# Kernel tuning notes

Measured on AMD Instinct MI355X. Metric: run time of the kernel, lower is better.

The kernel has to match this reference:

```python
import jax, jax.numpy as jnp
import numpy as np

L = 9  # local window size


def local_windows(x, l):
    # x: (n, c, h, w) -> (n, c, l*l, h, w): all l*l shifted views (zero-padded),
    # equivalent to F.unfold(x, kernel=(l,l), stride=1, padding=l//2).
    n, c, h, w = x.shape
    pad = l // 2
    xp = jnp.pad(x, ((0, 0), (0, 0), (pad, pad), (pad, pad)))
    views = [xp[:, :, i:i + h, j:j + w] for i in range(l) for j in range(l)]
    return jnp.stack(views, axis=2)


def setup_inputs() -> dict:
    key = jax.random.key(0)
    k1, k2, k3 = jax.random.split(key, 3)
    n, c, h, w = 2, 128, 64, 64
    ft = jax.random.normal(k1, (n, c, h, w), dtype=jnp.float32)
    fk = jax.random.normal(k2, (n, c, h, w), dtype=jnp.float32)
    # 1x1 conv weight shared between key and query projections: (out_c, in_c)
    W = jax.random.normal(k3, (128, 128), dtype=jnp.float32) * (1.0 / np.sqrt(128))
    return {"ft": ft, "fk": fk, "W": W}


def reference(ft, fk, W):
    # 1x1 conv == channel matmul
    key = jnp.einsum('oi,nihw->nohw', W, ft)    # key from frame t
    query = jnp.einsum('oi,nihw->nohw', W, fk)  # query from frame k
    # f_similar(query, key, L): per-pixel query dotted with L*L local keys
    key_win = local_windows(key, L)             # (n, c, L*L, h, w)
    sim = jnp.einsum('nchw,nckhw->nhwk', query, key_win)  # (n, h, w, L*L)
    weight = jax.nn.softmax(sim, axis=-1)
    # f_weighting(ft, weight, L): weighted sum of L*L local raw-ft vectors
    ft_win = local_windows(ft, L)                # (n, c, L*L, h, w)
    out = jnp.einsum('nckhw,nhwk->nchw', ft_win, weight)
    return out
```

## Files before the change

kernel.cpp:

```cpp
#include <hip/hip_runtime.h>
#include <hip/hip_bf16.h>


#define Hh 64
#define Ww 64
#define Cc 128
#define Nn 2
#define KK 81
#define HW (Hh * Ww)
#define CHW (Cc * HW)
#define P_TOT (Nn * HW)

typedef _Float16 h8 __attribute__((ext_vector_type(8)));
typedef _Float16 h4 __attribute__((ext_vector_type(4)));
typedef float f4v __attribute__((ext_vector_type(4)));

#ifndef __has_builtin
#define __has_builtin(x) 0
#endif

#if __has_builtin(__builtin_amdgcn_ds_read_tr16_b64_v4f16)
#define TR_BUILTIN 1
typedef __fp16 g4 __attribute__((__vector_size__(4 * sizeof(__fp16))));
static __device__ __forceinline__ h4 tr16(const _Float16* p) {
    g4 r = __builtin_amdgcn_ds_read_tr16_b64_v4f16(
        (__attribute__((address_space(3))) g4*)p);
    return __builtin_bit_cast(h4, r);
}
#else
#define TR_BUILTIN 0
static __device__ __forceinline__ h4 tr16(const _Float16* p) {
    h4 r;
    asm volatile("ds_read_b64_tr_b16 %0, %1"
                 : "=v"(r)
                 : "v"((__attribute__((address_space(3))) _Float16*)p));
    return r;
}
#endif

__global__ __launch_bounds__(256) void proj_kernel(const float* __restrict__ ft,
                                                   const float* __restrict__ fk,
                                                   const float* __restrict__ Wm,
                                                   _Float16* __restrict__ Qbuf,
                                                   _Float16* __restrict__ Kbuf,
                                                   _Float16* __restrict__ fth) {
    __shared__ __align__(16) _Float16 Wth[128 * 136];
    __shared__ __align__(16) _Float16 xkh[32 * 136];
    __shared__ __align__(16) _Float16 xqh[32 * 136];
    const int t = threadIdx.x;
    const int p0 = blockIdx.x * 32;
    const int nn = p0 >> 12;
    const int gbase = nn * CHW + (p0 & 4095);

#pragma unroll 4
    for (int e = t; e < 4096; e += 256) {
        const int n = e >> 5, ch = e & 31;
        const float4 v = *(const float4*)&Wm[n * 128 + (ch << 2)];
        h4 hv; hv[0] = (_Float16)v.x; hv[1] = (_Float16)v.y;
               hv[2] = (_Float16)v.z; hv[3] = (_Float16)v.w;
        *(h4*)&Wth[n * 136 + (ch << 2)] = hv;
    }
#pragma unroll 4
    for (int e = t; e < 1024; e += 256) {
        const int c = e >> 3, pc = e & 7;
        const float4 vk = *(const float4*)&ft[gbase + c * HW + (pc << 2)];
        const float4 vq = *(const float4*)&fk[gbase + c * HW + (pc << 2)];
        const int px = pc << 2;
        xkh[(px    ) * 136 + c] = (_Float16)vk.x;
        xkh[(px + 1) * 136 + c] = (_Float16)vk.y;
        xkh[(px + 2) * 136 + c] = (_Float16)vk.z;
        xkh[(px + 3) * 136 + c] = (_Float16)vk.w;
        xqh[(px    ) * 136 + c] = (_Float16)vq.x;
        xqh[(px + 1) * 136 + c] = (_Float16)vq.y;
        xqh[(px + 2) * 136 + c] = (_Float16)vq.z;
        xqh[(px + 3) * 136 + c] = (_Float16)vq.w;
    }
    __syncthreads();

#pragma unroll
    for (int e = t; e < 512; e += 256) {
        const int px = e >> 4, cq = e & 15;
        *(h8*)&fth[(size_t)(p0 + px) * 128 + (cq << 3)] =
            *(const h8*)&xkh[px * 136 + (cq << 3)];
    }

    const int lane = t & 63, wv = t >> 6;
    const int quad = lane >> 4, l15 = lane & 15;
    const _Float16* xs = (wv >> 1) ? xqh : xkh;
    _Float16* dst = (wv >> 1) ? Qbuf : Kbuf;
    const int mt = wv & 1;
    const int abase = (mt * 16 + l15) * 136 + (quad << 3);
    const h8 a0 = *(const h8*)&xs[abase];
    const h8 a1 = *(const h8*)&xs[abase + 32];
    const h8 a2 = *(const h8*)&xs[abase + 64];
    const h8 a3 = *(const h8*)&xs[abase + 96];
#pragma unroll
    for (int nt = 0; nt < 8; ++nt) {
        const int bbase = (nt * 16 + l15) * 136 + (quad << 3);
        const h8 b0 = *(const h8*)&Wth[bbase];
        const h8 b1 = *(const h8*)&Wth[bbase + 32];
        const h8 b2 = *(const h8*)&Wth[bbase + 64];
        const h8 b3 = *(const h8*)&Wth[bbase + 96];
        f4v acc = {0.f, 0.f, 0.f, 0.f};
        acc = __builtin_amdgcn_mfma_f32_16x16x32_f16(a0, b0, acc, 0, 0, 0);
        acc = __builtin_amdgcn_mfma_f32_16x16x32_f16(a1, b1, acc, 0, 0, 0);
        acc = __builtin_amdgcn_mfma_f32_16x16x32_f16(a2, b2, acc, 0, 0, 0);
        acc = __builtin_amdgcn_mfma_f32_16x16x32_f16(a3, b3, acc, 0, 0, 0);
        const int col = nt * 16 + l15;
        const size_t rb = (size_t)(p0 + mt * 16 + (quad << 2)) * 128 + col;
#pragma unroll
        for (int r = 0; r < 4; ++r)
            dst[rb + (size_t)r * 128] = (_Float16)acc[r];
    }
}

#define FTL_CH 2312
__global__ __launch_bounds__(256, 4) void sim_weight_kernel(const _Float16* __restrict__ Qbuf,
                                                            const _Float16* __restrict__ Kbuf,
                                                            const _Float16* __restrict__ fth,
                                                            float* __restrict__ out) {
    __shared__ __align__(16) unsigned char smem[40720];
    _Float16* Ksw  = (_Float16*)smem;
    _Float16* Qsw  = (_Float16*)(smem + 36864);
    _Float16* ftl  = (_Float16*)smem;
    float*    simbF= (float*)smem;
    _Float16* simb = (_Float16*)(smem + 39168);
    float*    redM = (float*)(smem + 40464);
    float*    redS = (float*)(smem + 40592);

    const int t  = threadIdx.x;
    const int b  = blockIdx.x;
    const int x0 = (b & 7) << 3;
    const int y  = (b >> 3) & 63;
    const int nn = b >> 9;
    const int pg0 = (nn << 12) + (y << 6) + x0;

#pragma unroll 3
    for (int e = t; e < 144 * 16; e += 256) {
        const int v = e >> 4, ci = e & 15;
        const int gx = x0 + (v & 15) - 4;
        const int gy = y + (v >> 4) - 4;
        h8 val = {0, 0, 0, 0, 0, 0, 0, 0};
        if ((unsigned)gx < 64u && (unsigned)gy < 64u)
            val = *(const h8*)&Kbuf[(size_t)((nn << 12) + (gy << 6) + gx) * 128 + (ci << 3)];
        *(h8*)&Ksw[(v << 7) + ((ci ^ (v & 15)) << 3)] = val;
    }
    if (t < 128) {
        const int v = t >> 4, ci = t & 15;
        *(h8*)&Qsw[(v << 7) + ((ci ^ v) << 3)] =
            *(const h8*)&Qbuf[(size_t)(pg0 + v) * 128 + (ci << 3)];
    }
    __syncthreads();

    h8 pf[9];
#pragma unroll
    for (int i = 0; i < 9; ++i) {
        const int e = t + (i << 8);
        const int v = e >> 4, ci = e & 15;
        const int gx = x0 + (v & 15) - 4;
        const int gy = y + (v >> 4) - 4;
        h8 val = {0, 0, 0, 0, 0, 0, 0, 0};
        if ((unsigned)gx < 64u && (unsigned)gy < 64u)
            val = *(const h8*)&fth[(size_t)((nn << 12) + (gy << 6) + gx) * 128 + (ci << 3)];
        pf[i] = val;
    }

    const int lane = t & 63, wv = t >> 6;
    const int quad = lane >> 4, l15 = lane & 15;
    const int qrow = l15 & 7;
    h8 qb[4];
#pragma unroll
    for (int kc = 0; kc < 4; ++kc) {
        const int ci = (kc << 2) + quad;
        qb[kc] = *(const h8*)&Qsw[(qrow << 7) + ((ci ^ qrow) << 3)];
    }
    const int r0 = wv, r1 = wv + 4;
    f4v acc0 = {0.f,0.f,0.f,0.f}, acc1 = acc0, acc2 = acc0;
#pragma unroll
    for (int kc = 0; kc < 4; ++kc) {
        const int ci = (kc << 2) + quad;
        const h8 kA = *(const h8*)&Ksw[(((r0 << 4) + l15) << 7) + ((ci ^ l15) << 3)];
        const h8 kB = *(const h8*)&Ksw[(((r1 << 4) + l15) << 7) + ((ci ^ l15) << 3)];
        const h8 kC = *(const h8*)&Ksw[(((8  << 4) + l15) << 7) + ((ci ^ l15) << 3)];
        acc0 = __builtin_amdgcn_mfma_f32_16x16x32_f16(kA, qb[kc], acc0, 0, 0, 0);
        acc1 = __builtin_amdgcn_mfma_f32_16x16x32_f16(kB, qb[kc], acc1, 0, 0, 0);
        acc2 = __builtin_amdgcn_mfma_f32_16x16x32_f16(kC, qb[kc], acc2, 0, 0, 0);
    }
    __syncthreads();

#pragma unroll
    for (int reg = 0; reg < 4; ++reg) {
        const int xx = (quad << 2) + reg;
        const int dx = xx - l15;
        const bool ok = (l15 < 8) && (dx >= 0) && (dx < 9);
        if (ok)            simbF[(r0 * 9 + dx) * 8 + l15] = acc0[reg];
        if (ok)            simbF[(r1 * 9 + dx) * 8 + l15] = acc1[reg];
        if (ok && wv == 0) simbF[(8  * 9 + dx) * 8 + l15] = acc2[reg];
    }
    __syncthreads();

    const int p = t & 7, kb = t >> 3;
    const bool has2 = (kb + 64 < KK);
    const float s0 = simbF[kb * 8 + p];
    const float s1 = simbF[(kb + 32) * 8 + p];
    const float s2 = has2 ? simbF[(kb + 64) * 8 + p] : 0.f;
    __syncthreads();

#pragma unroll
    for (int i = 0; i < 9; ++i) {
        const int e = t + (i << 8);
        const int v = e >> 4, ci = e & 15;
        *(h8*)&ftl[(ci >> 1) * FTL_CH + (v << 4) + ((ci & 1) << 3)] = pf[i];
    }

    float m = fmaxf(s0, s1);
    if (has2) m = fmaxf(m, s2);
#pragma unroll
    for (int off = 8; off <= 32; off <<= 1) m = fmaxf(m, __shfl_xor(m, off));
    if ((t & 56) == 0) redM[((t >> 6) << 3) + p] = m;
    __syncthreads();

    const _Float16* ftc0 = ftl + wv * FTL_CH;
    const _Float16* ftc1 = ftl + (wv + 4) * FTL_CH;
    h4 bfr[18];
#pragma unroll
    for (int r = 0; r < 9; ++r) {
        bfr[r]     = tr16(ftc0 + (r << 8) + (lane << 2));
        bfr[9 + r] = tr16(ftc1 + (r << 8) + (lane << 2));
    }

    float mm = fmaxf(fmaxf(redM[p], redM[8 + p]), fmaxf(redM[16 + p], redM[24 + p]));
    const float e0 = __expf(s0 - mm);
    const float e1 = __expf(s1 - mm);
    const float e2 = has2 ? __expf(s2 - mm) : 0.f;
    simb[kb * 8 + p] = (_Float16)e0;
    simb[(kb + 32) * 8 + p] = (_Float16)e1;
    if (has2) simb[(kb + 64) * 8 + p] = (_Float16)e2;
    float s = e0 + e1 + e2;
#pragma unroll
    for (int off = 8; off <= 32; off <<= 1) s += __shfl_xor(s, off);
    if ((t & 56) == 0) redS[((t >> 6) << 3) + p] = s;
    __syncthreads();

#if !TR_BUILTIN
    asm volatile("s_waitcnt lgkmcnt(0)");
    __builtin_amdgcn_sched_barrier(0);
#endif

    f4v aw0 = {0.f, 0.f, 0.f, 0.f}, aw1 = aw0;
#pragma unroll
    for (int r = 0; r < 9; ++r) {
        h4 afr;
#pragma unroll
        for (int j = 0; j < 4; ++j) {
            const int dx = (quad << 2) + j - qrow;
            const bool ok = (unsigned)dx < 9u;
            afr[j] = ok ? simb[(((r * 9 + dx) << 3) + qrow)] : (_Float16)0.f;
        }
        aw0 = __builtin_amdgcn_mfma_f32_16x16x16f16(afr, bfr[r],     aw0, 0, 0, 0);
        aw1 = __builtin_amdgcn_mfma_f32_16x16x16f16(afr, bfr[9 + r], aw1, 0, 0, 0);
    }

    if (quad < 2) {
        const int q4 = quad << 2;
        const float4 rs0 = *(const float4*)&redS[q4];
        const float4 rs1 = *(const float4*)&redS[8 + q4];
        const float4 rs2 = *(const float4*)&redS[16 + q4];
        const float4 rs3 = *(const float4*)&redS[24 + q4];
        const float iv0 = 1.f / (rs0.x + rs1.x + rs2.x + rs3.x);
        const float iv1 = 1.f / (rs0.y + rs1.y + rs2.y + rs3.y);
        const float iv2 = 1.f / (rs0.z + rs1.z + rs2.z + rs3.z);
        const float iv3 = 1.f / (rs0.w + rs1.w + rs2.w + rs3.w);
        const int xb = (y << 6) + x0 + q4;
        const size_t ob0 = ((size_t)((nn << 7) + (wv << 4) + l15) << 12) + xb;
        const size_t ob1 = ((size_t)((nn << 7) + ((wv + 4) << 4) + l15) << 12) + xb;
        float4 o0, o1;
        o0.x = aw0[0] * iv0; o0.y = aw0[1] * iv1; o0.z = aw0[2] * iv2; o0.w = aw0[3] * iv3;
        o1.x = aw1[0] * iv0; o1.y = aw1[1] * iv1; o1.z = aw1[2] * iv2; o1.w = aw1[3] * iv3;
        *(float4*)&out[ob0] = o0;
        *(float4*)&out[ob1] = o1;
    }
}

extern "C" void kernel_launch(void* const* d_in, const int* in_sizes, int n_in,
                              void* d_out, int out_size, void* d_ws, size_t ws_size,
                              hipStream_t stream) {
    const float* ft = (const float*)d_in[0];
    const float* fk = (const float*)d_in[1];
    const float* Wm = (const float*)d_in[2];
    float* out = (float*)d_out;

    _Float16* wsh  = (_Float16*)d_ws;
    _Float16* Qbuf = wsh;
    _Float16* Kbuf = wsh + 1048576;
    _Float16* fth  = wsh + 2097152;

    proj_kernel<<<256, 256, 0, stream>>>(ft, fk, Wm, Qbuf, Kbuf, fth);
    sim_weight_kernel<<<1024, 256, 0, stream>>>(Qbuf, Kbuf, fth, out);
}
```

Before: 77.25 us.

## Compute softmax from MFMA registers and halve projection tile per block

The similarity kernel now computes the softmax max and exp-sum straight from the MFMA accumulator registers, reducing across lanes with shuffles and a small cross-wave array. This drops the fp32 staging buffer and two block barriers. Separately, the projection kernel handles 16 pixels per block instead of 32 and splits output column tiles across waves, launching twice as many blocks to fill more CUs. The trade-off is that each projection block reloads the full weight matrix for half as much work.

```diff
diff --git a/kernel.cpp b/kernel.cpp
--- a/kernel.cpp
+++ b/kernel.cpp
@@ -45,10 +45,10 @@
                                                    _Float16* __restrict__ Kbuf,
                                                    _Float16* __restrict__ fth) {
     __shared__ __align__(16) _Float16 Wth[128 * 136];
-    __shared__ __align__(16) _Float16 xkh[32 * 136];
-    __shared__ __align__(16) _Float16 xqh[32 * 136];
+    __shared__ __align__(16) _Float16 xkh[16 * 136];
+    __shared__ __align__(16) _Float16 xqh[16 * 136];
     const int t = threadIdx.x;
-    const int p0 = blockIdx.x * 32;
+    const int p0 = blockIdx.x * 16;
     const int nn = p0 >> 12;
     const int gbase = nn * CHW + (p0 & 4095);
 
@@ -60,9 +60,9 @@
                hv[2] = (_Float16)v.z; hv[3] = (_Float16)v.w;
         *(h4*)&Wth[n * 136 + (ch << 2)] = hv;
     }
-#pragma unroll 4
-    for (int e = t; e < 1024; e += 256) {
-        const int c = e >> 3, pc = e & 7;
+#pragma unroll
+    for (int e = t; e < 512; e += 256) {
+        const int c = e >> 2, pc = e & 3;
         const float4 vk = *(const float4*)&ft[gbase + c * HW + (pc << 2)];
         const float4 vq = *(const float4*)&fk[gbase + c * HW + (pc << 2)];
         const int px = pc << 2;
@@ -77,9 +77,8 @@
     }
     __syncthreads();
 
-#pragma unroll
-    for (int e = t; e < 512; e += 256) {
-        const int px = e >> 4, cq = e & 15;
+    {
+        const int px = t >> 4, cq = t & 15;
         *(h8*)&fth[(size_t)(p0 + px) * 128 + (cq << 3)] =
             *(const h8*)&xkh[px * 136 + (cq << 3)];
     }
@@ -88,14 +87,15 @@
     const int quad = lane >> 4, l15 = lane & 15;
     const _Float16* xs = (wv >> 1) ? xqh : xkh;
     _Float16* dst = (wv >> 1) ? Qbuf : Kbuf;
-    const int mt = wv & 1;
-    const int abase = (mt * 16 + l15) * 136 + (quad << 3);
+    const int nt0 = (wv & 1) << 2;
+    const int abase = l15 * 136 + (quad << 3);
     const h8 a0 = *(const h8*)&xs[abase];
     const h8 a1 = *(const h8*)&xs[abase + 32];
     const h8 a2 = *(const h8*)&xs[abase + 64];
     const h8 a3 = *(const h8*)&xs[abase + 96];
 #pragma unroll
-    for (int nt = 0; nt < 8; ++nt) {
+    for (int ni = 0; ni < 4; ++ni) {
+        const int nt = nt0 + ni;
         const int bbase = (nt * 16 + l15) * 136 + (quad << 3);
         const h8 b0 = *(const h8*)&Wth[bbase];
         const h8 b1 = *(const h8*)&Wth[bbase + 32];
@@ -107,7 +107,7 @@
         acc = __builtin_amdgcn_mfma_f32_16x16x32_f16(a2, b2, acc, 0, 0, 0);
         acc = __builtin_amdgcn_mfma_f32_16x16x32_f16(a3, b3, acc, 0, 0, 0);
         const int col = nt * 16 + l15;
-        const size_t rb = (size_t)(p0 + mt * 16 + (quad << 2)) * 128 + col;
+        const size_t rb = (size_t)(p0 + (quad << 2)) * 128 + col;
 #pragma unroll
         for (int r = 0; r < 4; ++r)
             dst[rb + (size_t)r * 128] = (_Float16)acc[r];
@@ -123,7 +123,6 @@
     _Float16* Ksw  = (_Float16*)smem;
     _Float16* Qsw  = (_Float16*)(smem + 36864);
     _Float16* ftl  = (_Float16*)smem;
-    float*    simbF= (float*)smem;
     _Float16* simb = (_Float16*)(smem + 39168);
     float*    redM = (float*)(smem + 40464);
     float*    redS = (float*)(smem + 40592);
@@ -186,24 +185,20 @@
         acc1 = __builtin_amdgcn_mfma_f32_16x16x32_f16(kB, qb[kc], acc1, 0, 0, 0);
         acc2 = __builtin_amdgcn_mfma_f32_16x16x32_f16(kC, qb[kc], acc2, 0, 0, 0);
     }
-    __syncthreads();
-
+
+    float m = -3.0e38f;
 #pragma unroll
     for (int reg = 0; reg < 4; ++reg) {
-        const int xx = (quad << 2) + reg;
-        const int dx = xx - l15;
-        const bool ok = (l15 < 8) && (dx >= 0) && (dx < 9);
-        if (ok)            simbF[(r0 * 9 + dx) * 8 + l15] = acc0[reg];
-        if (ok)            simbF[(r1 * 9 + dx) * 8 + l15] = acc1[reg];
-        if (ok && wv == 0) simbF[(8  * 9 + dx) * 8 + l15] = acc2[reg];
-    }
-    __syncthreads();
-
-    const int p = t & 7, kb = t >> 3;
-    const bool has2 = (kb + 64 < KK);
-    const float s0 = simbF[kb * 8 + p];
-    const float s1 = simbF[(kb + 32) * 8 + p];
-    const float s2 = has2 ? simbF[(kb + 64) * 8 + p] : 0.f;
+        const int dx = (quad << 2) + reg - l15;
+        const bool ok = (l15 < 8) && ((unsigned)dx < 9u);
+        if (ok) {
+            m = fmaxf(m, fmaxf(acc0[reg], acc1[reg]));
+            m = fmaxf(m, acc2[reg]);
+        }
+    }
+    m = fmaxf(m, __shfl_xor(m, 16));
+    m = fmaxf(m, __shfl_xor(m, 32));
+    if (quad == 0 && l15 < 8) redM[(wv << 3) + l15] = m;
     __syncthreads();
 
 #pragma unroll
@@ -213,11 +208,24 @@
         *(h8*)&ftl[(ci >> 1) * FTL_CH + (v << 4) + ((ci & 1) << 3)] = pf[i];
     }
 
-    float m = fmaxf(s0, s1);
-    if (has2) m = fmaxf(m, s2);
-#pragma unroll
-    for (int off = 8; off <= 32; off <<= 1) m = fmaxf(m, __shfl_xor(m, off));
-    if ((t & 56) == 0) redM[((t >> 6) << 3) + p] = m;
+    const float mm = fmaxf(fmaxf(redM[qrow], redM[8 + qrow]),
+                           fmaxf(redM[16 + qrow], redM[24 + qrow]));
+    float ssum = 0.f;
+#pragma unroll
+    for (int reg = 0; reg < 4; ++reg) {
+        const int dx = (quad << 2) + reg - l15;
+        const bool ok = (l15 < 8) && ((unsigned)dx < 9u);
+        const float e0 = ok ? __expf(acc0[reg] - mm) : 0.f;
+        const float e1 = ok ? __expf(acc1[reg] - mm) : 0.f;
+        const float e2 = (ok && wv == 0) ? __expf(acc2[reg] - mm) : 0.f;
+        if (ok)            simb[((r0 * 9 + dx) << 3) + l15] = (_Float16)e0;
+        if (ok)            simb[((r1 * 9 + dx) << 3) + l15] = (_Float16)e1;
+        if (ok && wv == 0) simb[((8  * 9 + dx) << 3) + l15] = (_Float16)e2;
+        ssum += e0 + e1 + e2;
+    }
+    ssum += __shfl_xor(ssum, 16);
+    ssum += __shfl_xor(ssum, 32);
+    if (quad == 0 && l15 < 8) redS[(wv << 3) + l15] = ssum;
     __syncthreads();
 
     const _Float16* ftc0 = ftl + wv * FTL_CH;
@@ -228,19 +236,6 @@
         bfr[r]     = tr16(ftc0 + (r << 8) + (lane << 2));
         bfr[9 + r] = tr16(ftc1 + (r << 8) + (lane << 2));
     }
-
-    float mm = fmaxf(fmaxf(redM[p], redM[8 + p]), fmaxf(redM[16 + p], redM[24 + p]));
-    const float e0 = __expf(s0 - mm);
-    const float e1 = __expf(s1 - mm);
-    const float e2 = has2 ? __expf(s2 - mm) : 0.f;
-    simb[kb * 8 + p] = (_Float16)e0;
-    simb[(kb + 32) * 8 + p] = (_Float16)e1;
-    if (has2) simb[(kb + 64) * 8 + p] = (_Float16)e2;
-    float s = e0 + e1 + e2;
-#pragma unroll
-    for (int off = 8; off <= 32; off <<= 1) s += __shfl_xor(s, off);
-    if ((t & 56) == 0) redS[((t >> 6) << 3) + p] = s;
-    __syncthreads();
 
 #if !TR_BUILTIN
     asm volatile("s_waitcnt lgkmcnt(0)");
@@ -295,6 +290,6 @@
     _Float16* Kbuf = wsh + 1048576;
     _Float16* fth  = wsh + 2097152;
 
-    proj_kernel<<<256, 256, 0, stream>>>(ft, fk, Wm, Qbuf, Kbuf, fth);
+    proj_kernel<<<512, 256, 0, stream>>>(ft, fk, Wm, Qbuf, Kbuf, fth);
     sim_weight_kernel<<<1024, 256, 0, stream>>>(Qbuf, Kbuf, fth, out);
 }
```

Result: no change. 76.79 us (-0.6%).
